# Performance work log

Hardware: AMD Instinct MI355X
Metric: run time of the kernel (lower is better)

The kernel has to match this reference:

```python
import jax, jax.numpy as jnp
import numpy as np

N = 100_000      # num nodes
R = 7            # num relations
D = 64           # input_dim == output_dim
E = 1_600_000    # num edges
EDIM = 16        # edge_input_dim


def setup_inputs() -> dict:
    key = jax.random.key(0)
    ks = jax.random.split(key, 10)
    node_in = jax.random.randint(ks[0], (E,), 0, N)
    node_out = jax.random.randint(ks[1], (E,), 0, N)
    relation = jax.random.randint(ks[2], (E,), 0, R)
    edge_list = jnp.stack([node_in, node_out, relation], axis=1)  # (E, 3)
    x = jax.random.normal(ks[3], (N, D), dtype=jnp.float32)
    edge_weight = jax.random.uniform(ks[4], (E,), dtype=jnp.float32)
    edge_feature = jax.random.normal(ks[5], (E, EDIM), dtype=jnp.float32)
    s = 1.0 / np.sqrt(R * D)
    W_lin = jax.random.uniform(ks[6], (D, R * D), minval=-s, maxval=s, dtype=jnp.float32)
    b_lin = jnp.zeros((D,), jnp.float32)
    s2 = 1.0 / np.sqrt(D)
    W_self = jax.random.uniform(ks[7], (D, D), minval=-s2, maxval=s2, dtype=jnp.float32)
    b_self = jnp.zeros((D,), jnp.float32)
    s3 = 1.0 / np.sqrt(EDIM)
    W_edge = jax.random.uniform(ks[8], (D, EDIM), minval=-s3, maxval=s3, dtype=jnp.float32)
    b_edge = jnp.zeros((D,), jnp.float32)
    return {"x": x, "edge_list": edge_list, "edge_weight": edge_weight,
            "edge_feature": edge_feature, "W_lin": W_lin, "b_lin": b_lin,
            "W_self": W_self, "b_self": b_self, "W_edge": W_edge, "b_edge": b_edge}


def reference(x, edge_list, edge_weight, edge_feature, W_lin, b_lin, W_self, b_self, W_edge, b_edge):
    node_in, node_out, relation = edge_list[:, 0], edge_list[:, 1], edge_list[:, 2]
    # destination index in the flattened (node, relation) space
    seg = node_out * R + relation  # (E,)
    # sparse.mm(adj.T, x): scatter w * x[src] into (N*R, D)
    msg = edge_weight[:, None] * x[node_in]  # (E, D)
    update = jax.ops.segment_sum(msg, seg, num_segments=N * R)  # (N*R, D)
    # edge feature branch: edge_linear then weighted scatter_add
    edge_msg = (edge_feature @ W_edge.T + b_edge) * edge_weight[:, None]  # (E, D)
    update = update + jax.ops.segment_sum(edge_msg, seg, num_segments=N * R)
    update = update.reshape(N, R * D)
    out = update @ W_lin.T + b_lin + x @ W_self.T + b_self
    return jax.nn.relu(out)
```

## Files before the change

### kernel.cpp

```cpp
#include <hip/hip_runtime.h>
#include <hip/hip_bf16.h>
#include <hip/hip_fp16.h>

#define N_NODES 100000
#define R_REL   7
#define E_EDGES 1600000
#define EDIM    16
#define KTOT    640
#define KSTR    648
#define CAP     56

typedef __bf16 bf16_t;
typedef bf16_t bf16x8 __attribute__((ext_vector_type(8)));
typedef bf16_t bf16x4 __attribute__((ext_vector_type(4)));
typedef float  f32x4  __attribute__((ext_vector_type(4)));
typedef unsigned long long u64;

#define RFL(v) __builtin_amdgcn_readfirstlane(v)
#define RL(v, l) __builtin_amdgcn_readlane(v, l)


__device__ __forceinline__ void sc1(int e, int src, int dst, int rel, float w,
                                    int* __restrict__ cnt, u64* __restrict__ recs8) {
    unsigned wb = __float_as_uint(w) & 0xFFFFFE00u;
    int slot = atomicAdd(&cnt[dst], 1);
    unsigned u0 = (unsigned)src | ((unsigned)rel << 17) | ((unsigned)(e & 0xFFF) << 20);
    unsigned u1 = ((unsigned)e >> 12) | wb;
    recs8[(size_t)dst * CAP + slot] = ((u64)u1 << 32) | u0;
}

__global__ __launch_bounds__(256) void k_pre(
    const float* __restrict__ x, const int* __restrict__ el,
    const float* __restrict__ wgt,
    const float* __restrict__ W_lin, const float* __restrict__ W_self,
    const float* __restrict__ W_edge, const float* __restrict__ b_edge,
    int* __restrict__ cnt, bf16_t* __restrict__ xb, bf16_t* __restrict__ Bp,
    u64* __restrict__ recs8)
{
    const int t = blockIdx.x * 256 + threadIdx.x;

    if (t < (N_NODES * 64) / 16) {
        const float4* xp = (const float4*)(x + (size_t)t * 16);
        float4 v0 = xp[0], v1 = xp[1], v2 = xp[2], v3 = xp[3];
        bf16x8 o0 = {(bf16_t)v0.x, (bf16_t)v0.y, (bf16_t)v0.z, (bf16_t)v0.w,
                     (bf16_t)v1.x, (bf16_t)v1.y, (bf16_t)v1.z, (bf16_t)v1.w};
        bf16x8 o1 = {(bf16_t)v2.x, (bf16_t)v2.y, (bf16_t)v2.z, (bf16_t)v2.w,
                     (bf16_t)v3.x, (bf16_t)v3.y, (bf16_t)v3.z, (bf16_t)v3.w};
        *(bf16x8*)(xb + (size_t)t * 16)     = o0;
        *(bf16x8*)(xb + (size_t)t * 16 + 8) = o1;
    }

    if (t < KTOT * 64) {
        int k = t >> 6;
        int j = t & 63;
        float v;
        if (k < 448) {
            v = W_lin[j * 448 + k];
        } else if (k < 512) {
            v = W_self[j * 64 + (k - 448)];
        } else if (k < 624) {
            int r = (k - 512) >> 4, kk = (k - 512) & 15;
            float sacc = 0.f;
            for (int d = 0; d < 64; d++)
                sacc = fmaf(W_lin[j * 448 + r * 64 + d], W_edge[d * 16 + kk], sacc);
            v = sacc;
        } else if (k < 631) {
            int r = k - 624;
            float sacc = 0.f;
            for (int d = 0; d < 64; d++)
                sacc = fmaf(W_lin[j * 448 + r * 64 + d], b_edge[d], sacc);
            v = sacc;
        } else {
            v = 0.f;
        }
        Bp[((k >> 3) * 64 + j) * 8 + (k & 7)] = (bf16_t)v;
    }

    if (t < E_EDGES / 4) {
        const int4* ep = (const int4*)(el + (size_t)t * 12);
        int4 q0 = ep[0], q1 = ep[1], q2 = ep[2];
        float4 w4 = *(const float4*)(wgt + (size_t)t * 4);
        int e = t * 4;
        sc1(e + 0, q0.x, q0.y, q0.z, w4.x, cnt, recs8);
        sc1(e + 1, q0.w, q1.x, q1.y, w4.y, cnt, recs8);
        sc1(e + 2, q1.z, q1.w, q2.x, w4.z, cnt, recs8);
        sc1(e + 3, q2.y, q2.z, q2.w, w4.w, cnt, recs8);
    }
}


__global__ __launch_bounds__(256) void k_main(
    const bf16_t* __restrict__ xb, const float* __restrict__ ef,
    const float* __restrict__ b_lin, const float* __restrict__ b_self,
    const int* __restrict__ cnt, const u64* __restrict__ recs8,
    const bf16_t* __restrict__ Bp, float* __restrict__ out)
{
    __shared__ __align__(16) bf16_t A[16 * KSTR];
    const int wave = threadIdx.x >> 6;
    const int lane = threadIdx.x & 63;
    const int lef  = lane & 15;
    const int nodeBase = blockIdx.x * 16;
    const int n0 = nodeBase + wave * 4;

    const int4 m4 = *(const int4*)(cnt + n0);
    u64    rw[4];
    bf16_t sv[4];
#pragma unroll
    for (int i = 0; i < 4; i++) {
        rw[i] = recs8[(size_t)(n0 + i) * CAP + min(lane, CAP - 1)];
        sv[i] = xb[(n0 + i) * 64 + lane];
    }

#pragma unroll
    for (int i = 0; i < 4; i++) {
        const int row = wave * 4 + i;
        bf16_t* Ar = A + row * KSTR;
        Ar[448 + lane] = sv[i];
        if (lane < 9) Ar[631 + lane] = (bf16_t)0.f;

        int m = (i == 0) ? m4.x : (i == 1) ? m4.y : (i == 2) ? m4.z : m4.w;
        m = min(m, CAP);
        const unsigned u0v = (unsigned)rw[i];
        const unsigned u1v = (unsigned)(rw[i] >> 32);
        const int  relv  = (u0v >> 17) & 7;
        const bool valid = lane < m;

        for (int r = 0; r < R_REL; r++) {
            u64 mr = __ballot(valid && (relv == r));
            float a = 0.f, F = 0.f, s = 0.f;
            while (mr) {
                int i0 = __builtin_ctzll(mr); mr &= mr - 1;
                int i1 = i0; bool two = false, more = false;
                if (mr) { i1 = __builtin_ctzll(mr); mr &= mr - 1;
                          two = true; more = (mr != 0); }
                unsigned a0 = RL(u0v, i0), b0 = RL(u1v, i0);
                unsigned a1 = RL(u0v, i1), b1 = RL(u1v, i1);
                int src0 = a0 & 0x1FFFF, src1 = a1 & 0x1FFFF;
                int e0 = (a0 >> 20) | ((b0 & 0x1FF) << 12);
                int e1 = (a1 >> 20) | ((b1 & 0x1FF) << 12);
                float w0 = __uint_as_float(b0 & 0xFFFFFE00u);
                float w1 = two ? __uint_as_float(b1 & 0xFFFFFE00u) : 0.f;
                float xv0 = (float)xb[src0 * 64 + lane];
                float xv1 = (float)xb[src1 * 64 + lane];
                float ev0 = ef[e0 * EDIM + lef];
                float ev1 = ef[e1 * EDIM + lef];
                if (more) {
                    int i2 = __builtin_ctzll(mr); mr &= mr - 1;
                    int i3 = i2; bool four = false;
                    if (mr) { i3 = __builtin_ctzll(mr); mr &= mr - 1; four = true; }
                    unsigned a2 = RL(u0v, i2), b2 = RL(u1v, i2);
                    unsigned a3 = RL(u0v, i3), b3 = RL(u1v, i3);
                    int src2 = a2 & 0x1FFFF, src3 = a3 & 0x1FFFF;
                    int e2 = (a2 >> 20) | ((b2 & 0x1FF) << 12);
                    int e3 = (a3 >> 20) | ((b3 & 0x1FF) << 12);
                    float w2 = __uint_as_float(b2 & 0xFFFFFE00u);
                    float w3 = four ? __uint_as_float(b3 & 0xFFFFFE00u) : 0.f;
                    float xv2 = (float)xb[src2 * 64 + lane];
                    float xv3 = (float)xb[src3 * 64 + lane];
                    float ev2 = ef[e2 * EDIM + lef];
                    float ev3 = ef[e3 * EDIM + lef];
                    a = fmaf(w2, xv2, a); F = fmaf(w2, ev2, F); s += w2;
                    a = fmaf(w3, xv3, a); F = fmaf(w3, ev3, F); s += w3;
                }
                a = fmaf(w0, xv0, a); F = fmaf(w0, ev0, F); s += w0;
                a = fmaf(w1, xv1, a); F = fmaf(w1, ev1, F); s += w1;
            }
            Ar[r * 64 + lane] = (bf16_t)a;
            if (lane < EDIM) Ar[512 + r * EDIM + lane] = (bf16_t)F;
            if (lane == 0)   Ar[624 + r] = (bf16_t)s;
        }
    }
    __syncthreads();

    const int quad = lane >> 4;
    const int l15  = lane & 15;
    f32x4 c = {0.f, 0.f, 0.f, 0.f};
#pragma unroll
    for (int s2i = 0; s2i < KTOT / 32; s2i++) {
        bf16x8 a = *(const bf16x8*)(A + l15 * KSTR + s2i * 32 + quad * 8);
        bf16x8 b = *(const bf16x8*)(Bp + (((s2i * 4 + quad) * 64) + wave * 16 + l15) * 8);
        c = __builtin_amdgcn_mfma_f32_16x16x32_bf16(a, b, c, 0, 0, 0);
    }
    const int j = wave * 16 + l15;
    const float bias = b_lin[j] + b_self[j];
#pragma unroll
    for (int q = 0; q < 4; q++) {
        const int n = nodeBase + quad * 4 + q;
        float v = c[q] + bias;
        out[n * 64 + j] = v > 0.f ? v : 0.f;
    }
}


extern "C" void kernel_launch(void* const* d_in, const int* in_sizes, int n_in,
                              void* d_out, int out_size, void* d_ws, size_t ws_size,
                              hipStream_t stream) {
    const float* x      = (const float*)d_in[0];
    const int*   el     = (const int*)  d_in[1];
    const float* wgt    = (const float*)d_in[2];
    const float* ef     = (const float*)d_in[3];
    const float* W_lin  = (const float*)d_in[4];
    const float* b_lin  = (const float*)d_in[5];
    const float* W_self = (const float*)d_in[6];
    const float* b_self = (const float*)d_in[7];
    const float* W_edge = (const float*)d_in[8];
    const float* b_edge = (const float*)d_in[9];
    float* out = (float*)d_out;

    u64*    recs8 = (u64*)d_ws;
    int*    cnt   = (int*)(recs8 + (size_t)N_NODES * CAP);
    bf16_t* xb    = (bf16_t*)(cnt + N_NODES);
    bf16_t* Bp    = xb + (size_t)N_NODES * 64;

    hipMemsetAsync(cnt, 0, N_NODES * sizeof(int), stream);
    k_pre <<<1563, 256, 0, stream>>>(x, el, wgt, W_lin, W_self, W_edge, b_edge,
                                     cnt, xb, Bp, recs8);
    k_main<<<N_NODES / 16, 256, 0, stream>>>(xb, ef, b_lin, b_self,
                                             cnt, recs8, Bp, out);
}
```

Baseline: 388.1 us.

## Use one wave per node in gather kernel and batch edge-bucketing atomics

The main kernel now launches 1024-thread blocks, so each of the 16 waves gathers a single node instead of each of 4 waves handling four nodes in sequence. This gives more parallel latency hiding for the random gathers, and only 4 waves then run the MFMA projection. The pre-pass now has each thread handle 8 edges, issuing all atomics before the record writes and storing records with nontemporal stores. The trade-off is 12 waves sitting idle during the MFMA phase and higher register and occupancy pressure from the larger blocks.

After: 426.5 us. +9.9%, slower.

```diff
diff --git a/kernel.cpp b/kernel.cpp
--- a/kernel.cpp
+++ b/kernel.cpp
@@ -19,15 +19,6 @@
 #define RFL(v) __builtin_amdgcn_readfirstlane(v)
 #define RL(v, l) __builtin_amdgcn_readlane(v, l)
 
-
-__device__ __forceinline__ void sc1(int e, int src, int dst, int rel, float w,
-                                    int* __restrict__ cnt, u64* __restrict__ recs8) {
-    unsigned wb = __float_as_uint(w) & 0xFFFFFE00u;
-    int slot = atomicAdd(&cnt[dst], 1);
-    unsigned u0 = (unsigned)src | ((unsigned)rel << 17) | ((unsigned)(e & 0xFFF) << 20);
-    unsigned u1 = ((unsigned)e >> 12) | wb;
-    recs8[(size_t)dst * CAP + slot] = ((u64)u1 << 32) | u0;
-}
 
 __global__ __launch_bounds__(256) void k_pre(
     const float* __restrict__ x, const int* __restrict__ el,
@@ -76,20 +67,35 @@
         Bp[((k >> 3) * 64 + j) * 8 + (k & 7)] = (bf16_t)v;
     }
 
-    if (t < E_EDGES / 4) {
-        const int4* ep = (const int4*)(el + (size_t)t * 12);
+    if (t < E_EDGES / 8) {
+        const int4* ep = (const int4*)(el + (size_t)t * 24);
         int4 q0 = ep[0], q1 = ep[1], q2 = ep[2];
-        float4 w4 = *(const float4*)(wgt + (size_t)t * 4);
-        int e = t * 4;
-        sc1(e + 0, q0.x, q0.y, q0.z, w4.x, cnt, recs8);
-        sc1(e + 1, q0.w, q1.x, q1.y, w4.y, cnt, recs8);
-        sc1(e + 2, q1.z, q1.w, q2.x, w4.z, cnt, recs8);
-        sc1(e + 3, q2.y, q2.z, q2.w, w4.w, cnt, recs8);
+        int4 q3 = ep[3], q4 = ep[4], q5 = ep[5];
+        float4 wa = *(const float4*)(wgt + (size_t)t * 8);
+        float4 wc = *(const float4*)(wgt + (size_t)t * 8 + 4);
+        const int e = t * 8;
+        const int srcs[8] = {q0.x, q0.w, q1.z, q2.y, q3.x, q3.w, q4.z, q5.y};
+        const int dsts[8] = {q0.y, q1.x, q1.w, q2.z, q3.y, q4.x, q4.w, q5.z};
+        const int rels[8] = {q0.z, q1.y, q2.x, q2.w, q3.z, q4.y, q5.x, q5.w};
+        const float ws[8] = {wa.x, wa.y, wa.z, wa.w, wc.x, wc.y, wc.z, wc.w};
+        int slot[8];
+#pragma unroll
+        for (int i = 0; i < 8; i++)
+            slot[i] = atomicAdd(&cnt[dsts[i]], 1);
+#pragma unroll
+        for (int i = 0; i < 8; i++) {
+            unsigned u0 = (unsigned)srcs[i] | ((unsigned)rels[i] << 17)
+                        | ((unsigned)((e + i) & 0xFFF) << 20);
+            unsigned u1 = ((unsigned)(e + i) >> 12)
+                        | (__float_as_uint(ws[i]) & 0xFFFFFE00u);
+            __builtin_nontemporal_store(((u64)u1 << 32) | u0,
+                &recs8[(size_t)dsts[i] * CAP + slot[i]]);
+        }
     }
 }
 
 
-__global__ __launch_bounds__(256) void k_main(
+__global__ __launch_bounds__(1024) void k_main(
     const bf16_t* __restrict__ xb, const float* __restrict__ ef,
     const float* __restrict__ b_lin, const float* __restrict__ b_self,
     const int* __restrict__ cnt, const u64* __restrict__ recs8,
@@ -100,94 +106,86 @@
     const int lane = threadIdx.x & 63;
     const int lef  = lane & 15;
     const int nodeBase = blockIdx.x * 16;
-    const int n0 = nodeBase + wave * 4;
-
-    const int4 m4 = *(const int4*)(cnt + n0);
-    u64    rw[4];
-    bf16_t sv[4];
-#pragma unroll
-    for (int i = 0; i < 4; i++) {
-        rw[i] = recs8[(size_t)(n0 + i) * CAP + min(lane, CAP - 1)];
-        sv[i] = xb[(n0 + i) * 64 + lane];
-    }
-
-#pragma unroll
-    for (int i = 0; i < 4; i++) {
-        const int row = wave * 4 + i;
-        bf16_t* Ar = A + row * KSTR;
-        Ar[448 + lane] = sv[i];
-        if (lane < 9) Ar[631 + lane] = (bf16_t)0.f;
-
-        int m = (i == 0) ? m4.x : (i == 1) ? m4.y : (i == 2) ? m4.z : m4.w;
-        m = min(m, CAP);
-        const unsigned u0v = (unsigned)rw[i];
-        const unsigned u1v = (unsigned)(rw[i] >> 32);
-        const int  relv  = (u0v >> 17) & 7;
-        const bool valid = lane < m;
-
-        for (int r = 0; r < R_REL; r++) {
-            u64 mr = __ballot(valid && (relv == r));
-            float a = 0.f, F = 0.f, s = 0.f;
-            while (mr) {
-                int i0 = __builtin_ctzll(mr); mr &= mr - 1;
-                int i1 = i0; bool two = false, more = false;
-                if (mr) { i1 = __builtin_ctzll(mr); mr &= mr - 1;
-                          two = true; more = (mr != 0); }
-                unsigned a0 = RL(u0v, i0), b0 = RL(u1v, i0);
-                unsigned a1 = RL(u0v, i1), b1 = RL(u1v, i1);
-                int src0 = a0 & 0x1FFFF, src1 = a1 & 0x1FFFF;
-                int e0 = (a0 >> 20) | ((b0 & 0x1FF) << 12);
-                int e1 = (a1 >> 20) | ((b1 & 0x1FF) << 12);
-                float w0 = __uint_as_float(b0 & 0xFFFFFE00u);
-                float w1 = two ? __uint_as_float(b1 & 0xFFFFFE00u) : 0.f;
-                float xv0 = (float)xb[src0 * 64 + lane];
-                float xv1 = (float)xb[src1 * 64 + lane];
-                float ev0 = ef[e0 * EDIM + lef];
-                float ev1 = ef[e1 * EDIM + lef];
-                if (more) {
-                    int i2 = __builtin_ctzll(mr); mr &= mr - 1;
-                    int i3 = i2; bool four = false;
-                    if (mr) { i3 = __builtin_ctzll(mr); mr &= mr - 1; four = true; }
-                    unsigned a2 = RL(u0v, i2), b2 = RL(u1v, i2);
-                    unsigned a3 = RL(u0v, i3), b3 = RL(u1v, i3);
-                    int src2 = a2 & 0x1FFFF, src3 = a3 & 0x1FFFF;
-                    int e2 = (a2 >> 20) | ((b2 & 0x1FF) << 12);
-                    int e3 = (a3 >> 20) | ((b3 & 0x1FF) << 12);
-                    float w2 = __uint_as_float(b2 & 0xFFFFFE00u);
-                    float w3 = four ? __uint_as_float(b3 & 0xFFFFFE00u) : 0.f;
-                    float xv2 = (float)xb[src2 * 64 + lane];
-                    float xv3 = (float)xb[src3 * 64 + lane];
-                    float ev2 = ef[e2 * EDIM + lef];
-                    float ev3 = ef[e3 * EDIM + lef];
-                    a = fmaf(w2, xv2, a); F = fmaf(w2, ev2, F); s += w2;
-                    a = fmaf(w3, xv3, a); F = fmaf(w3, ev3, F); s += w3;
-                }
-                a = fmaf(w0, xv0, a); F = fmaf(w0, ev0, F); s += w0;
-                a = fmaf(w1, xv1, a); F = fmaf(w1, ev1, F); s += w1;
+    const int n = nodeBase + wave;
+
+    const int m = min(cnt[n], CAP);
+    u64 rv = 0;
+    if (lane < m) rv = recs8[(size_t)n * CAP + lane];
+    const bf16_t svv = xb[n * 64 + lane];
+
+    bf16_t* Ar = A + wave * KSTR;
+    Ar[448 + lane] = svv;
+    if (lane < 9) Ar[631 + lane] = (bf16_t)0.f;
+
+    const unsigned u0v = (unsigned)rv;
+    const unsigned u1v = (unsigned)(rv >> 32);
+    const int  relv  = (u0v >> 17) & 7;
+    const bool valid = lane < m;
+
+    for (int r = 0; r < R_REL; r++) {
+        u64 mr = __ballot(valid && (relv == r));
+        float a = 0.f, F = 0.f, s = 0.f;
+        while (mr) {
+            int i0 = __builtin_ctzll(mr); mr &= mr - 1;
+            int i1 = i0; bool two = false, more = false;
+            if (mr) { i1 = __builtin_ctzll(mr); mr &= mr - 1;
+                      two = true; more = (mr != 0); }
+            unsigned a0 = RL(u0v, i0), b0 = RL(u1v, i0);
+            unsigned a1 = RL(u0v, i1), b1 = RL(u1v, i1);
+            int src0 = a0 & 0x1FFFF, src1 = a1 & 0x1FFFF;
+            int e0 = (a0 >> 20) | ((b0 & 0x1FF) << 12);
+            int e1 = (a1 >> 20) | ((b1 & 0x1FF) << 12);
+            float w0 = __uint_as_float(b0 & 0xFFFFFE00u);
+            float w1 = two ? __uint_as_float(b1 & 0xFFFFFE00u) : 0.f;
+            float xv0 = (float)xb[src0 * 64 + lane];
+            float xv1 = (float)xb[src1 * 64 + lane];
+            float ev0 = ef[e0 * EDIM + lef];
+            float ev1 = ef[e1 * EDIM + lef];
+            if (more) {
+                int i2 = __builtin_ctzll(mr); mr &= mr - 1;
+                int i3 = i2; bool four = false;
+                if (mr) { i3 = __builtin_ctzll(mr); mr &= mr - 1; four = true; }
+                unsigned a2 = RL(u0v, i2), b2 = RL(u1v, i2);
+                unsigned a3 = RL(u0v, i3), b3 = RL(u1v, i3);
+                int src2 = a2 & 0x1FFFF, src3 = a3 & 0x1FFFF;
+                int e2 = (a2 >> 20) | ((b2 & 0x1FF) << 12);
+                int e3 = (a3 >> 20) | ((b3 & 0x1FF) << 12);
+                float w2 = __uint_as_float(b2 & 0xFFFFFE00u);
+                float w3 = four ? __uint_as_float(b3 & 0xFFFFFE00u) : 0.f;
+                float xv2 = (float)xb[src2 * 64 + lane];
+                float xv3 = (float)xb[src3 * 64 + lane];
+                float ev2 = ef[e2 * EDIM + lef];
+                float ev3 = ef[e3 * EDIM + lef];
+                a = fmaf(w2, xv2, a); F = fmaf(w2, ev2, F); s += w2;
+                a = fmaf(w3, xv3, a); F = fmaf(w3, ev3, F); s += w3;
             }
-            Ar[r * 64 + lane] = (bf16_t)a;
-            if (lane < EDIM) Ar[512 + r * EDIM + lane] = (bf16_t)F;
-            if (lane == 0)   Ar[624 + r] = (bf16_t)s;
-        }
+            a = fmaf(w0, xv0, a); F = fmaf(w0, ev0, F); s += w0;
+            a = fmaf(w1, xv1, a); F = fmaf(w1, ev1, F); s += w1;
+        }
+        Ar[r * 64 + lane] = (bf16_t)a;
+        if (lane < EDIM) Ar[512 + r * EDIM + lane] = (bf16_t)F;
+        if (lane == 0)   Ar[624 + r] = (bf16_t)s;
     }
     __syncthreads();
 
-    const int quad = lane >> 4;
-    const int l15  = lane & 15;
-    f32x4 c = {0.f, 0.f, 0.f, 0.f};
-#pragma unroll
-    for (int s2i = 0; s2i < KTOT / 32; s2i++) {
-        bf16x8 a = *(const bf16x8*)(A + l15 * KSTR + s2i * 32 + quad * 8);
-        bf16x8 b = *(const bf16x8*)(Bp + (((s2i * 4 + quad) * 64) + wave * 16 + l15) * 8);
-        c = __builtin_amdgcn_mfma_f32_16x16x32_bf16(a, b, c, 0, 0, 0);
-    }
-    const int j = wave * 16 + l15;
-    const float bias = b_lin[j] + b_self[j];
-#pragma unroll
-    for (int q = 0; q < 4; q++) {
-        const int n = nodeBase + quad * 4 + q;
-        float v = c[q] + bias;
-        out[n * 64 + j] = v > 0.f ? v : 0.f;
+    if (wave < 4) {
+        const int quad = lane >> 4;
+        const int l15  = lane & 15;
+        f32x4 c = {0.f, 0.f, 0.f, 0.f};
+#pragma unroll
+        for (int s2i = 0; s2i < KTOT / 32; s2i++) {
+            bf16x8 av = *(const bf16x8*)(A + l15 * KSTR + s2i * 32 + quad * 8);
+            bf16x8 bv = *(const bf16x8*)(Bp + (((s2i * 4 + quad) * 64) + wave * 16 + l15) * 8);
+            c = __builtin_amdgcn_mfma_f32_16x16x32_bf16(av, bv, c, 0, 0, 0);
+        }
+        const int j = wave * 16 + l15;
+        const float bias = b_lin[j] + b_self[j];
+#pragma unroll
+        for (int q = 0; q < 4; q++) {
+            const int nn = nodeBase + quad * 4 + q;
+            float v = c[q] + bias;
+            out[nn * 64 + j] = v > 0.f ? v : 0.f;
+        }
     }
 }
 
@@ -215,6 +213,6 @@
     hipMemsetAsync(cnt, 0, N_NODES * sizeof(int), stream);
     k_pre <<<1563, 256, 0, stream>>>(x, el, wgt, W_lin, W_self, W_edge, b_edge,
                                      cnt, xb, Bp, recs8);
-    k_main<<<N_NODES / 16, 256, 0, stream>>>(xb, ef, b_lin, b_self,
-                                             cnt, recs8, Bp, out);
+    k_main<<<N_NODES / 16, 1024, 0, stream>>>(xb, ef, b_lin, b_self,
+                                              cnt, recs8, Bp, out);
 }
```
